# Kernel tuning notes

Measured on AMD Instinct MI355X. Metric: run time of the kernel, lower is better.

## Reference

```python
import jax, jax.numpy as jnp
import numpy as np
from jax import lax

C = 64
KD = 16  # in_channels // k_factor
KS = 3
DN = ('NCHW', 'OIHW', 'NCHW')


def setup_inputs() -> dict:
    key = jax.random.key(0)
    ks = jax.random.split(key, 9)
    B, H, W = 4, 128, 128
    s = 0.05
    return {
        'x': jax.random.normal(ks[0], (B, C, H, W), jnp.float32),
        'y': jax.random.normal(ks[1], (B, C, H, W), jnp.float32),
        'z': jax.random.normal(ks[2], (B, C, H, W), jnp.float32),
        'Wq': jax.random.normal(ks[3], (C, 1, KS, KS), jnp.float32) * s,   # depthwise
        'bq': jax.random.normal(ks[4], (C,), jnp.float32) * s,
        'Wk': jax.random.normal(ks[5], (KD, C, KS, KS), jnp.float32) * s,
        'bk': jax.random.normal(ks[6], (KD,), jnp.float32) * s,
        'wv': jax.random.normal(ks[7], (KD,), jnp.float32) * s,           # 1x1 conv 1->KD
        'bv': jax.random.normal(ks[8], (KD,), jnp.float32) * s,
    }


def reference(x, y, z, Wq, bq, Wk, bk, wv, bv):
    # Q: depthwise 3x3 conv + ReLU on y -> [B,C,H,W]
    q = jax.nn.relu(
        lax.conv_general_dilated(y, Wq, (1, 1), 'SAME',
                                 dimension_numbers=DN, feature_group_count=C)
        + bq[None, :, None, None])
    # K: 3x3 conv C->KD + ReLU on x -> [B,KD,H,W], shared across the C channel axis
    k = jax.nn.relu(
        lax.conv_general_dilated(x, Wk, (1, 1), 'SAME', dimension_numbers=DN)
        + bk[None, :, None, None])
    # V: 1x1 conv 1->KD + ReLU applied per input channel of z -> [B,C,KD,H,W]
    v = jax.nn.relu(z[:, :, None] * wv[None, None, :, None, None]
                    + bv[None, None, :, None, None])
    # Degenerate SDPA: head_dim=1 so scale=1; softmax over the KD 'sequence' axis.
    scores = q[:, :, None] * k[:, None]              # [B,C,KD,H,W]
    attn = jax.nn.softmax(scores, axis=2)
    return jnp.sum(attn * v, axis=2)                 # [B,C,H,W]
```

## Files before the change

kernel.cpp:

```cpp
#include <hip/hip_runtime.h>

#define HH 128
#define WW 128
#define CC 64
#define KD 16
#define HW (HH * WW)
#define HWB (HW * 4)
#define TOTBYTES (4u * CC * HW * 4u)
#define OOB_SENT 0x40000000

typedef __attribute__((ext_vector_type(4))) int   int32x4_t;
typedef __attribute__((ext_vector_type(4))) float floatx4;

__device__ floatx4 llvm_amdgcn_raw_buffer_load_v4f32(int32x4_t srsrc, int voffset,
                                                     int soffset, int aux)
    __asm("llvm.amdgcn.raw.buffer.load.v4f32");
__device__ float llvm_amdgcn_raw_buffer_load_f32(int32x4_t srsrc, int voffset,
                                                 int soffset, int aux)
    __asm("llvm.amdgcn.raw.buffer.load.f32");

__device__ inline int32x4_t make_srd(const void* p, unsigned bytes) {
    const unsigned long long a = (unsigned long long)p;
    int32x4_t r;
    r.x = (int)(a & 0xffffffffull);
    r.y = (int)(a >> 32);
    r.z = (int)bytes;
    r.w = 0x00020000;
    return r;
}

#if __has_builtin(__builtin_amdgcn_exp2f)
#define FAST_EXP2(x) __builtin_amdgcn_exp2f(x)
#define KLOG2E 1.44269504088896340736f
#else
#define FAST_EXP2(x) __expf(x)
#define KLOG2E 1.0f
#endif

__global__ __launch_bounds__(512, 8) void gatev_fused(
    const float* __restrict__ x, const float* __restrict__ y,
    const float* __restrict__ z,
    const float* __restrict__ Wq, const float* __restrict__ bq,
    const float* __restrict__ Wk, const float* __restrict__ bk,
    const float* __restrict__ wv, const float* __restrict__ bv,
    float* __restrict__ out)
{
    __shared__ float wk_lds[9216];

    const int tid  = threadIdx.x;
    const int g    = __builtin_amdgcn_readfirstlane(tid >> 6);
    const int lane = tid & 63;
    const int px   = lane & 15, py = lane >> 4;
    const int b    = blockIdx.z;
    const int h    = blockIdx.y * 4 + py;
    const int w    = blockIdx.x * 16 + px;
    const int pix  = h * WW + w;

    const int32x4_t rx = make_srd(x, TOTBYTES);
    const int32x4_t ry = make_srd(y, TOTBYTES);
    const int32x4_t rz = make_srd(z, TOTBYTES);

    const int colb = (w > 0 ? w - 1 : 0) * 4;
    int rowB[3];
#pragma unroll
    for (int r = 0; r < 3; ++r) {
        const int rr = h - 1 + r;
        rowB[r] = (rr >= 0 && rr < HH) ? rr * WW * 4 + colb : OOB_SENT;
    }
    const float mL = (w > 0) ? 1.f : 0.f;
    const float mR = (w < WW - 1) ? 1.f : 0.f;
    const bool  w0e = (w == 0);

    const int base = b * CC * HWB;
    const int c0   = __builtin_amdgcn_readfirstlane(g * 8);

#pragma unroll
    for (int p = 0; p < 18; ++p) {
        const int s   = p * 512 + tid;
        const int d   = s / 576;
        const int rem = s - d * 576;
        const int c   = rem / 9;
        const int t   = rem - c * 9;
        wk_lds[(c >> 3) * 1152 + (c & 7) * 144 + d * 9 + t] = Wk[s];
    }
    __syncthreads();

    float acc[KD];
#pragma unroll
    for (int d = 0; d < KD; ++d) acc[d] = 0.f;

    auto load3 = [&](floatx4 (&f)[3], int so) {
#pragma unroll
        for (int r = 0; r < 3; ++r)
            f[r] = llvm_amdgcn_raw_buffer_load_v4f32(rx, rowB[r], so, 0);
    };
    auto compute = [&](const floatx4 (&f)[3], int wb) {
        float tp[9];
#pragma unroll
        for (int r = 0; r < 3; ++r) {
            tp[r * 3 + 0] = f[r].x * mL;
            tp[r * 3 + 1] = w0e ? f[r].x : f[r].y;
            tp[r * 3 + 2] = (w0e ? f[r].y : f[r].z) * mR;
        }
#pragma unroll
        for (int i = 0; i < 36; ++i) {
            const floatx4 wf = *(const floatx4*)&wk_lds[wb + i * 4];
#pragma unroll
            for (int j = 0; j < 4; ++j) {
                const int flat = i * 4 + j;
                acc[flat / 9] = fmaf(wf[j], tp[flat % 9], acc[flat / 9]);
            }
        }
    };

    const int wbase = g * 1152;
    floatx4 f0[3], f1[3];
    load3(f0, base + c0 * HWB);
#pragma unroll
    for (int cp = 0; cp < 4; ++cp) {
        load3(f1, base + (c0 + 2 * cp + 1) * HWB);
        compute(f0, wbase + (2 * cp) * 144);
        load3(f0, base + (c0 + 2 * cp + 2) * HWB);
        compute(f1, wbase + (2 * cp + 1) * 144);
    }
    __syncthreads();

#pragma unroll
    for (int d = 0; d < KD; ++d)
        wk_lds[g * (KD * 64) + d * 64 + lane] = acc[d];
    __syncthreads();

#pragma unroll
    for (int rep = 0; rep < 2; ++rep) {
        const int idx = tid + rep * 512;
        float s = wk_lds[idx];
#pragma unroll
        for (int gg = 1; gg < 8; ++gg) s += wk_lds[gg * (KD * 64) + idx];
        const int d = idx >> 6;
        wk_lds[idx] = fmaxf(s + bk[d], 0.f) * KLOG2E;
    }
    __syncthreads();

    float qv[8], zv[8];
#pragma unroll 2
    for (int ci = 0; ci < 8; ++ci) {
        const int c  = c0 + ci;
        const int so = base + c * HWB;
        const float* wq = Wq + c * 9;
        float a = 0.f;
#pragma unroll
        for (int r = 0; r < 3; ++r) {
            const floatx4 f = llvm_amdgcn_raw_buffer_load_v4f32(ry, rowB[r], so, 0);
            const float tL = f.x * mL;
            const float tC = w0e ? f.x : f.y;
            const float tR = (w0e ? f.y : f.z) * mR;
            a = fmaf(wq[r * 3 + 0], tL, a);
            a = fmaf(wq[r * 3 + 1], tC, a);
            a = fmaf(wq[r * 3 + 2], tR, a);
        }
        qv[ci] = fmaxf(a + bq[c], 0.f);
        zv[ci] = llvm_amdgcn_raw_buffer_load_f32(rz, pix * 4, so, 0);
    }

    float num[8], den[8];
#pragma unroll
    for (int ci = 0; ci < 8; ++ci) { num[ci] = 0.f; den[ci] = 0.f; }

#pragma unroll
    for (int d = 0; d < KD; ++d) {
        const float kl  = wk_lds[d * 64 + lane];
        const float wvd = wv[d];
        const float bvd = bv[d];
#pragma unroll
        for (int ci = 0; ci < 8; ++ci) {
            const float e = FAST_EXP2(qv[ci] * kl);
            const float v = fmaxf(zv[ci] * wvd + bvd, 0.f);
            num[ci] = fmaf(e, v, num[ci]);
            den[ci] += e;
        }
    }

    float* ob = out + (size_t)b * CC * HW;
#pragma unroll
    for (int ci = 0; ci < 8; ++ci)
        ob[(c0 + ci) * HW + pix] = __fdividef(num[ci], den[ci]);
}

extern "C" void kernel_launch(void* const* d_in, const int* in_sizes, int n_in,
                              void* d_out, int out_size, void* d_ws, size_t ws_size,
                              hipStream_t stream) {
    const float* x  = (const float*)d_in[0];
    const float* y  = (const float*)d_in[1];
    const float* z  = (const float*)d_in[2];
    const float* Wq = (const float*)d_in[3];
    const float* bq = (const float*)d_in[4];
    const float* Wk = (const float*)d_in[5];
    const float* bk = (const float*)d_in[6];
    const float* wv = (const float*)d_in[7];
    const float* bv = (const float*)d_in[8];
    float* out = (float*)d_out;

    dim3 grid(WW / 16, HH / 4, 4);
    dim3 block(512);
    hipLaunchKernelGGL(gatev_fused, grid, block, 0, stream,
                       x, y, z, Wq, bq, Wk, bk, wv, bv, out);
}
```

Measured before the change: 48.51 us.

## Use packed FP32 FMA for conv and softmax, skip edge masking in interior blocks

Reorders the K-conv weights in LDS to tap-major, output-channel-minor order so each tap can feed packed two-wide FMAs (v_pk_fma_f32) across output channels. The softmax/value accumulation is also vectorised into float2 pairs. Blocks away from the image edges take a uniform branch that skips the boundary mask multiplies and selects. The aim is to cut VALU instruction count in a compute-heavy fused kernel, at the cost of a branch and possible register-pressure changes.

```diff
diff --git a/kernel.cpp b/kernel.cpp
--- a/kernel.cpp
+++ b/kernel.cpp
@@ -11,6 +11,7 @@
 
 typedef __attribute__((ext_vector_type(4))) int   int32x4_t;
 typedef __attribute__((ext_vector_type(4))) float floatx4;
+typedef __attribute__((ext_vector_type(2))) float floatx2;
 
 __device__ floatx4 llvm_amdgcn_raw_buffer_load_v4f32(int32x4_t srsrc, int voffset,
                                                      int soffset, int aux)
@@ -56,6 +57,9 @@
     const int w    = blockIdx.x * 16 + px;
     const int pix  = h * WW + w;
 
+    const bool interior = (blockIdx.x > 0) & (blockIdx.x < 7) &
+                          (blockIdx.y > 0) & (blockIdx.y < 31);
+
     const int32x4_t rx = make_srd(x, TOTBYTES);
     const int32x4_t ry = make_srd(y, TOTBYTES);
     const int32x4_t rz = make_srd(z, TOTBYTES);
@@ -81,35 +85,39 @@
         const int rem = s - d * 576;
         const int c   = rem / 9;
         const int t   = rem - c * 9;
-        wk_lds[(c >> 3) * 1152 + (c & 7) * 144 + d * 9 + t] = Wk[s];
-    }
-    __syncthreads();
-
-    float acc[KD];
-#pragma unroll
-    for (int d = 0; d < KD; ++d) acc[d] = 0.f;
+        wk_lds[(c >> 3) * 1152 + (c & 7) * 144 + t * 16 + d] = Wk[s];
+    }
+    __syncthreads();
+
+    floatx2 acc2[8];
+#pragma unroll
+    for (int p = 0; p < 8; ++p) acc2[p] = (floatx2){0.f, 0.f};
 
     auto load3 = [&](floatx4 (&f)[3], int so) {
 #pragma unroll
         for (int r = 0; r < 3; ++r)
             f[r] = llvm_amdgcn_raw_buffer_load_v4f32(rx, rowB[r], so, 0);
     };
+    auto taps3 = [&](const floatx4& f, float& tL, float& tC, float& tR) {
+        if (interior) { tL = f.x; tC = f.y; tR = f.z; }
+        else {
+            tL = f.x * mL;
+            tC = w0e ? f.x : f.y;
+            tR = (w0e ? f.y : f.z) * mR;
+        }
+    };
     auto compute = [&](const floatx4 (&f)[3], int wb) {
         float tp[9];
 #pragma unroll
-        for (int r = 0; r < 3; ++r) {
-            tp[r * 3 + 0] = f[r].x * mL;
-            tp[r * 3 + 1] = w0e ? f[r].x : f[r].y;
-            tp[r * 3 + 2] = (w0e ? f[r].y : f[r].z) * mR;
-        }
-#pragma unroll
-        for (int i = 0; i < 36; ++i) {
-            const floatx4 wf = *(const floatx4*)&wk_lds[wb + i * 4];
-#pragma unroll
-            for (int j = 0; j < 4; ++j) {
-                const int flat = i * 4 + j;
-                acc[flat / 9] = fmaf(wf[j], tp[flat % 9], acc[flat / 9]);
-            }
+        for (int r = 0; r < 3; ++r)
+            taps3(f[r], tp[r * 3 + 0], tp[r * 3 + 1], tp[r * 3 + 2]);
+#pragma unroll
+        for (int t = 0; t < 9; ++t) {
+            const floatx2 tp2 = {tp[t], tp[t]};
+            const floatx2* wrow = (const floatx2*)&wk_lds[wb + t * 16];
+#pragma unroll
+            for (int p = 0; p < 8; ++p)
+                acc2[p] = __builtin_elementwise_fma(wrow[p], tp2, acc2[p]);
         }
     };
 
@@ -126,8 +134,10 @@
     __syncthreads();
 
 #pragma unroll
-    for (int d = 0; d < KD; ++d)
-        wk_lds[g * (KD * 64) + d * 64 + lane] = acc[d];
+    for (int p = 0; p < 8; ++p) {
+        wk_lds[g * 1024 + (2 * p + 0) * 64 + lane] = acc2[p].x;
+        wk_lds[g * 1024 + (2 * p + 1) * 64 + lane] = acc2[p].y;
+    }
     __syncthreads();
 
 #pragma unroll
@@ -135,13 +145,13 @@
         const int idx = tid + rep * 512;
         float s = wk_lds[idx];
 #pragma unroll
-        for (int gg = 1; gg < 8; ++gg) s += wk_lds[gg * (KD * 64) + idx];
+        for (int gg = 1; gg < 8; ++gg) s += wk_lds[gg * 1024 + idx];
         const int d = idx >> 6;
         wk_lds[idx] = fmaxf(s + bk[d], 0.f) * KLOG2E;
     }
     __syncthreads();
 
-    float qv[8], zv[8];
+    floatx2 qp[4], zp[4];
 #pragma unroll 2
     for (int ci = 0; ci < 8; ++ci) {
         const int c  = c0 + ci;
@@ -151,39 +161,45 @@
 #pragma unroll
         for (int r = 0; r < 3; ++r) {
             const floatx4 f = llvm_amdgcn_raw_buffer_load_v4f32(ry, rowB[r], so, 0);
-            const float tL = f.x * mL;
-            const float tC = w0e ? f.x : f.y;
-            const float tR = (w0e ? f.y : f.z) * mR;
+            float tL, tC, tR;
+            taps3(f, tL, tC, tR);
             a = fmaf(wq[r * 3 + 0], tL, a);
             a = fmaf(wq[r * 3 + 1], tC, a);
             a = fmaf(wq[r * 3 + 2], tR, a);
         }
-        qv[ci] = fmaxf(a + bq[c], 0.f);
-        zv[ci] = llvm_amdgcn_raw_buffer_load_f32(rz, pix * 4, so, 0);
-    }
-
-    float num[8], den[8];
-#pragma unroll
-    for (int ci = 0; ci < 8; ++ci) { num[ci] = 0.f; den[ci] = 0.f; }
+        qp[ci >> 1][ci & 1] = fmaxf(a + bq[c], 0.f);
+        zp[ci >> 1][ci & 1] = llvm_amdgcn_raw_buffer_load_f32(rz, pix * 4, so, 0);
+    }
+
+    floatx2 num2[4], den2[4];
+    const floatx2 zero2 = {0.f, 0.f};
+#pragma unroll
+    for (int p = 0; p < 4; ++p) { num2[p] = zero2; den2[p] = zero2; }
 
 #pragma unroll
     for (int d = 0; d < KD; ++d) {
         const float kl  = wk_lds[d * 64 + lane];
-        const float wvd = wv[d];
-        const float bvd = bv[d];
-#pragma unroll
-        for (int ci = 0; ci < 8; ++ci) {
-            const float e = FAST_EXP2(qv[ci] * kl);
-            const float v = fmaxf(zv[ci] * wvd + bvd, 0.f);
-            num[ci] = fmaf(e, v, num[ci]);
-            den[ci] += e;
+        const floatx2 kl2 = {kl, kl};
+        const float wvd = wv[d], bvd = bv[d];
+        const floatx2 wv2 = {wvd, wvd}, bv2 = {bvd, bvd};
+#pragma unroll
+        for (int p = 0; p < 4; ++p) {
+            const floatx2 s2 = qp[p] * kl2;
+            floatx2 e2;
+            e2.x = FAST_EXP2(s2.x);
+            e2.y = FAST_EXP2(s2.y);
+            const floatx2 v2 = __builtin_elementwise_max(
+                __builtin_elementwise_fma(zp[p], wv2, bv2), zero2);
+            num2[p] = __builtin_elementwise_fma(e2, v2, num2[p]);
+            den2[p] = den2[p] + e2;
         }
     }
 
     float* ob = out + (size_t)b * CC * HW;
 #pragma unroll
     for (int ci = 0; ci < 8; ++ci)
-        ob[(c0 + ci) * HW + pix] = __fdividef(num[ci], den[ci]);
+        ob[(c0 + ci) * HW + pix] =
+            __fdividef(num2[ci >> 1][ci & 1], den2[ci >> 1][ci & 1]);
 }
 
 extern "C" void kernel_launch(void* const* d_in, const int* in_sizes, int n_in,
```

After: 52.65 us. 8.6% more time.
